# Performance work log

Measured on AMD Instinct MI355X. Metric: run time of the kernel, lower is better.

The kernel has to match this reference:

```python
import jax, jax.numpy as jnp
import numpy as np

H = 1024      # hidden_dim
NH = 16       # num_heads
HD = H // NH  # head_dim
FF = 4096     # ff_dim
EPS = 1e-6


def layer_norm(x, gamma, beta):
    # faithful to source: unbiased std (ddof=1), divide by (std + eps)
    mean = jnp.mean(x, axis=-1, keepdims=True)
    var = jnp.sum((x - mean) ** 2, axis=-1, keepdims=True) / (x.shape[-1] - 1)
    std = jnp.sqrt(var)
    return gamma * (x - mean) / (std + EPS) + beta


def linear_mulbias(x, W, b):
    # source LinearLayer: einsum('...i,io,o->...o') -> (x @ W) * b (bias MULTIPLIES)
    return jnp.einsum('bti,io->bto', x, W) * b


def setup_inputs() -> dict:
    key = jax.random.key(0)
    ks = jax.random.split(key, 11)
    B, T = 2, 2048
    return {
        'x':      jax.random.normal(ks[0], (B, T, H), jnp.float32),
        'Wqkv':   jax.random.normal(ks[1], (H, 3 * H), jnp.float32),
        'bqkv':   jax.random.normal(ks[2], (3 * H,), jnp.float32),
        'W1':     jax.random.normal(ks[3], (H, FF), jnp.float32),
        'b1':     jax.random.normal(ks[4], (FF,), jnp.float32),
        'W2':     jax.random.normal(ks[5], (FF, H), jnp.float32),
        'b2':     jax.random.normal(ks[6], (H,), jnp.float32),
        'gamma1': jax.random.normal(ks[7], (H,), jnp.float32),
        'beta1':  jax.random.normal(ks[8], (H,), jnp.float32),
        'gamma2': jax.random.normal(ks[9], (H,), jnp.float32),
        'beta2':  jax.random.normal(ks[10], (H,), jnp.float32),
    }


def attention(x, Wqkv, bqkv):
    B, T, _ = x.shape
    qkv = linear_mulbias(x, Wqkv, bqkv)                 # [B,T,3H]
    # einops 'b t (d k h) -> k b h t d' with k=3, h=NH: last dim decomposes (d,3,h)
    qkv = qkv.reshape(B, T, HD, 3, NH)
    qkv = jnp.transpose(qkv, (3, 0, 4, 1, 2))           # [3,B,NH,T,HD]
    q, k, v = qkv[0], qkv[1], qkv[2]
    scores = jnp.einsum('bhid,bhjd->bhij', q, k) / (H ** 0.5)  # scale by full hidden_dim
    attn = jax.nn.softmax(scores, axis=-1)
    out = jnp.einsum('bhij,bhjd->bhid', attn, v)        # [B,NH,T,HD]
    return jnp.transpose(out, (0, 2, 1, 3)).reshape(B, T, H)


def reference(x, Wqkv, bqkv, W1, b1, W2, b2, gamma1, beta1, gamma2, beta2):
    # dropout is identity in eval mode
    out = layer_norm(x + attention(x, Wqkv, bqkv), gamma1, beta1)
    ffn = linear_mulbias(jnp.maximum(linear_mulbias(out, W1, b1), 0.0), W2, b2)
    out = layer_norm(out + ffn, gamma2, beta2)
    return out
```

## Files before the change

kernel.cpp:

```cpp
#include <hip/hip_runtime.h>
#include <math.h>

#define B 2
#define T 2048
#define H 1024
#define NH 16
#define HD 64
#define FF 4096
#define M_TOK (B*T)
#define LOG2E 1.4426950408889634f

typedef unsigned short u16;
typedef __attribute__((ext_vector_type(8))) short bf16x8;
typedef __attribute__((ext_vector_type(4))) float f32x4;

#define WAITBAR4  asm volatile("s_waitcnt vmcnt(4)\n\ts_barrier" ::: "memory")
#define WAITBAR6  asm volatile("s_waitcnt vmcnt(6)\n\ts_barrier" ::: "memory")
#define WAITBAR0  asm volatile("s_waitcnt vmcnt(0)\n\ts_barrier" ::: "memory")

__device__ __forceinline__ u16 f2bf(float f) {
  union { float f; unsigned u; } v; v.f = f;
  const unsigned r = (v.u + 0x7FFFu + ((v.u >> 16) & 1u)) >> 16;
  return (u16)r;
}
__device__ __forceinline__ float bf2f(u16 h) {
  union { unsigned u; float f; } v; v.u = ((unsigned)h) << 16;
  return v.f;
}
__device__ __forceinline__ unsigned cvt_pk_bf16(float lo, float hi) {
  unsigned r;
  asm("v_cvt_pk_bf16_f32 %0, %1, %2" : "=v"(r) : "v"(lo), "v"(hi));
  return r;
}
__device__ __forceinline__ float m3(float a, float b, float c) {
  return fmaxf(fmaxf(a, b), c);
}
__device__ __forceinline__ void gload16(const u16* g, u16* l) {
  __builtin_amdgcn_global_load_lds(
      (const __attribute__((address_space(1))) unsigned int*)g,
      (__attribute__((address_space(3))) unsigned int*)l, 16, 0, 0);
}

__global__ __launch_bounds__(256) void split_hl(
    const float* __restrict__ in, u16* __restrict__ oh, u16* __restrict__ ol)
{
  const size_t i = ((size_t)blockIdx.x * 256 + threadIdx.x) * 4;
  const float4 v = *(const float4*)(in + i);
  union { u16 s[4]; uint2 u; } h, l;
  const float f[4] = {v.x, v.y, v.z, v.w};
#pragma unroll
  for (int j = 0; j < 4; ++j) {
    const u16 hb = f2bf(f[j]); h.s[j] = hb; l.s[j] = f2bf(f[j] - bf2f(hb));
  }
  *(uint2*)(oh + i) = h.u;
  *(uint2*)(ol + i) = l.u;
}

template<int SPLIT>
__global__ __launch_bounds__(256) void transpose_bf16(
    const float* __restrict__ in, u16* __restrict__ oh, u16* __restrict__ ol,
    int K, int N)
{
  __shared__ float tile[64][69];
  const int k0 = blockIdx.y * 64, n0 = blockIdx.x * 64;
  const int tid = threadIdx.x;
  const int r = tid >> 4, c4 = (tid & 15) * 4;
#pragma unroll
  for (int i = 0; i < 4; ++i) {
    const float4 v = *(const float4*)(in + (size_t)(k0 + i*16 + r) * N + n0 + c4);
    tile[i*16+r][c4]   = v.x; tile[i*16+r][c4+1] = v.y;
    tile[i*16+r][c4+2] = v.z; tile[i*16+r][c4+3] = v.w;
  }
  __syncthreads();
  const int n = tid >> 2, kq = tid & 3;
  union { u16 s[8]; int4 v; } ph0, ph1, pl0, pl1;
#pragma unroll
  for (int j = 0; j < 8; ++j) {
    const float f0 = tile[kq*16 + j][n];
    const float f1 = tile[kq*16 + 8 + j][n];
    const u16 h0 = f2bf(f0), h1 = f2bf(f1);
    ph0.s[j] = h0; ph1.s[j] = h1;
    if (SPLIT) { pl0.s[j] = f2bf(f0 - bf2f(h0)); pl1.s[j] = f2bf(f1 - bf2f(h1)); }
  }
  u16* po = oh + (size_t)(n0 + n) * K + k0 + kq * 16;
  *(int4*)po = ph0.v; *(int4*)(po + 8) = ph1.v;
  if (SPLIT) {
    u16* pl = ol + (size_t)(n0 + n) * K + k0 + kq * 16;
    *(int4*)pl = pl0.v; *(int4*)(pl + 8) = pl1.v;
  }
}

__device__ __forceinline__ int swz(int r, int kq) {
  return r * 32 + ((kq ^ ((r >> 1) & 3)) * 8);
}

template<int SPLIT, int RELU, int OBF, int QKV3, int DEEP3, int PARTIAL>
__global__ __launch_bounds__(256) void mfma_gemm(
    const u16* __restrict__ Ah, const u16* __restrict__ Al,
    const u16* __restrict__ Bh, const u16* __restrict__ Bl,
    const float* __restrict__ bias,
// ... 114 lines not shown
      }
      __syncthreads();
      cur = nxt;
    }
  }
#undef GSTAGE
#undef BLSTAGE

  const int orow0 = row0 + wr * 64, ocol0 = col0 + wc * 64;
#pragma unroll
  for (int n = 0; n < 4; ++n) {
    const int col = ocol0 + n * 16 + fr;
    const float bs = PARTIAL ? 1.0f : bias[col];
#pragma unroll
    for (int m = 0; m < 4; ++m) {
      const int rbase = orow0 + m * 16 + (lane >> 4) * 4;
#pragma unroll
      for (int j = 0; j < 4; ++j) {
        float v = acc[m][n][j] * bs;
        if (RELU) v = fmaxf(v, 0.0f);
        const size_t off = (size_t)(rbase + j) * N + col;
        if (OBF) Cb[off] = f2bf(v); else Cf[off] = v;
      }
    }
  }
}

__global__ __launch_bounds__(256) void repack_qkv(
    const float* __restrict__ qkv,
    u16* __restrict__ Qh, u16* __restrict__ Ql,
    u16* __restrict__ Kh, u16* __restrict__ Kl, u16* __restrict__ Vb)
{
  const int bt = blockIdx.x;
  const int b = bt >> 11, t = bt & (T - 1);
  const int tid = threadIdx.x;
  __shared__ float Ls[3 * H];
  const float* src = qkv + (size_t)bt * (3 * H);
#pragma unroll
  for (int i = 0; i < 3; ++i) {
    const int c4 = i * 256 + tid;
    *(float4*)&Ls[c4 * 4] = *(const float4*)(src + c4 * 4);
  }
  __syncthreads();
  const float qscale = LOG2E / 32.0f;
#pragma unroll
  for (int i = 0; i < 4; ++i) {
    const int j = i * 256 + tid;
    const int h = j >> 6, d = j & 63;
    const size_t dst = (((size_t)(b * NH + h)) * T + t) * HD + d;
    const float q = Ls[d * 48 + h] * qscale;
    const u16 qhb = f2bf(q);
    Qh[dst] = qhb; Ql[dst] = f2bf(q - bf2f(qhb));
    const float k = Ls[d * 48 + 16 + h];
    const u16 khb = f2bf(k);
    Kh[dst] = khb; Kl[dst] = f2bf(k - bf2f(khb));
    Vb[dst] = f2bf(Ls[d * 48 + 32 + h]);
  }
}

__global__ __launch_bounds__(256) void vtrans(
    const u16* __restrict__ Vb, u16* __restrict__ VT)
{
  __shared__ u16 Ls[64][72];
  const int bh = blockIdx.y, t0 = blockIdx.x * 64;
  const int tid = threadIdx.x;
  const int r = tid >> 2, c = (tid & 3) * 16;
  const size_t src = ((size_t)bh * T + t0 + r) * HD + c;
  *(int4*)&Ls[r][c]     = *(const int4*)(Vb + src);
  *(int4*)&Ls[r][c + 8] = *(const int4*)(Vb + src + 8);
  __syncthreads();
  const int d = tid >> 2, tc = (tid & 3) * 16;
  u16 buf[16];
#pragma unroll
  for (int i = 0; i < 16; ++i) buf[i] = Ls[tc + i][d];
  u16* dst = VT + ((size_t)bh * HD + d) * T + t0 + tc;
  *(int4*)dst       = *(int4*)&buf[0];
  *(int4*)(dst + 8) = *(int4*)&buf[8];
}

__device__ __forceinline__ int sigma_k(int r) {
  return ((r >> 5) << 5) | (((r >> 2) & 3) << 3) | (((r >> 4) & 1) << 2) | (r & 3);
}

__global__ __launch_bounds__(256) void flash_attn_mfma(
    const u16* __restrict__ Qh, const u16* __restrict__ Ql,
    const u16* __restrict__ Kh, const u16* __restrict__ Kl,
    const u16* __restrict__ VT, float* __restrict__ Out)
{
  __shared__ u16 sm[3 * 12288];
  const int i = blockIdx.x;
  const int slot = i >> 3;
  const int bh = (i & 7) * 4 + (slot >> 4);
  const int row0 = (slot & 15) * 128;
  const int b = bh >> 4, h = bh & 15;
  const int tid = threadIdx.x, wave = tid >> 6, lane = tid & 63;
  const int fr = lane & 15, kq = lane >> 4;

  bf16x8 qh[2][2], ql[2][2];
#pragma unroll
  for (int qf = 0; qf < 2; ++qf) {
    const size_t qoff = ((size_t)bh * T + row0 + wave*32 + qf*16 + fr) * HD + kq*8;
#pragma unroll
    for (int ks = 0; ks < 2; ++ks) {
      qh[qf][ks] = *(const bf16x8*)(Qh + qoff + ks*32);
      ql[qf][ks] = *(const bf16x8*)(Ql + qoff + ks*32);
    }
  }

  bf16x8 ones8;
#pragma unroll
  for (int z = 0; z < 8; ++z) ones8[z] = (short)0x3F80;

  f32x4 o[2][4] = {};
  f32x4 oex[2] = {};
  float m_[2] = {-1e30f, -1e30f};

  const int c_ = wave * 2;
  const int r0_ = c_ * 8 + (lane >> 3), s_ = lane & 7;
  const int r1_ = r0_ + 8;
  const int cd0 = s_ ^ (r0_ & 7), cd1 = s_ ^ (r1_ & 7);
  const int k0_ = sigma_k(r0_), k1_ = sigma_k(r1_);
  const u16* pKh0 = Kh + ((size_t)bh*T + k0_)*HD + cd0*8;
  const u16* pKh1 = Kh + ((size_t)bh*T + k1_)*HD + cd1*8;
  const u16* pKl0 = Kl + ((size_t)bh*T + k0_)*HD + cd0*8;
  const u16* pKl1 = Kl + ((size_t)bh*T + k1_)*HD + cd1*8;
  const u16* pV0  = VT + ((size_t)bh*HD + r0_)*T + cd0*8;
  const u16* pV1  = VT + ((size_t)bh*HD + r1_)*T + cd1*8;

#define FSTAGE(sb) do { \
    gload16(pKh0, &sm[(sb) + c_*512]);        gload16(pKh1, &sm[(sb) + (c_+1)*512]); \
    gload16(pKl0, &sm[(sb) + 4096 + c_*512]); gload16(pKl1, &sm[(sb) + 4096 + (c_+1)*512]); \
    gload16(pV0,  &sm[(sb) + 8192 + c_*512]); gload16(pV1,  &sm[(sb) + 8192 + (c_+1)*512]); \
    pKh0 += 64*HD; pKh1 += 64*HD; pKl0 += 64*HD; pKl1 += 64*HD; pV0 += 64; pV1 += 64; \
  } while (0)

  FSTAGE(0);
  FSTAGE(12288);
  WAITBAR6;
  int cslot = 0, islot = 2;

  const int NT = T / 64;
  for (int t = 0; t < NT; ++t) {
    if (t + 2 < NT) {
      FSTAGE(islot * 12288);
      islot = (islot == 2) ? 0 : islot + 1;
    }
    const u16* smb = &sm[cslot * 12288];

    f32x4 s[2][4] = {};
    __builtin_amdgcn_s_setprio(1);
#pragma unroll
    for (int ks = 0; ks < 2; ++ks) {
#pragma unroll
      for (int n = 0; n < 4; ++n) {
        const int kr = n * 16 + fr;
        const int sl = ((ks*4 + kq) ^ (kr & 7)) * 8;
        const bf16x8 kh_ = *(const bf16x8*)&smb[kr*64 + sl];
        const bf16x8 kl_ = *(const bf16x8*)&smb[4096 + kr*64 + sl];
        s[0][n] = __builtin_amdgcn_mfma_f32_16x16x32_bf16(kh_, qh[0][ks], s[0][n], 0, 0, 0);
        s[1][n] = __builtin_amdgcn_mfma_f32_16x16x32_bf16(kh_, qh[1][ks], s[1][n], 0, 0, 0);
        s[0][n] = __builtin_amdgcn_mfma_f32_16x16x32_bf16(kl_, qh[0][ks], s[0][n], 0, 0, 0);
        s[1][n] = __builtin_amdgcn_mfma_f32_16x16x32_bf16(kl_, qh[1][ks], s[1][n], 0, 0, 0);
        s[0][n] = __builtin_amdgcn_mfma_f32_16x16x32_bf16(kh_, ql[0][ks], s[0][n], 0, 0, 0);
        s[1][n] = __builtin_amdgcn_mfma_f32_16x16x32_bf16(kh_, ql[1][ks], s[1][n], 0, 0, 0);
      }
    }
    __builtin_amdgcn_s_setprio(0);

    bf16x8 vf[2][4];
#pragma unroll
    for (int ks = 0; ks < 2; ++ks)
#pragma unroll
      for (int n = 0; n < 4; ++n) {
        const int dr = n * 16 + fr;
        vf[ks][n] = *(const bf16x8*)&smb[8192 + dr*64 + (((ks*4 + kq) ^ (dr & 7)) * 8)];
      }

#pragma unroll
    for (int qf = 0; qf < 2; ++qf) {
      const float g0 = m3(s[qf][0][0], s[qf][0][1], s[qf][0][2]);
      const float g1 = m3(s[qf][0][3], s[qf][1][0], s[qf][1][1]);
      const float g2 = m3(s[qf][1][2], s[qf][1][3], s[qf][2][0]);
      const float g3 = m3(s[qf][2][1], s[qf][2][2], s[qf][2][3]);
      const float g4 = m3(s[qf][3][0], s[qf][3][1], s[qf][3][2]);
      float mx = fmaxf(m3(g0, g1, g2), m3(g3, g4, s[qf][3][3]));
      mx = fmaxf(mx, __shfl_xor(mx, 16));
      mx = fmaxf(mx, __shfl_xor(mx, 32));
      if (!__all(mx <= m_[qf] + 8.0f)) {
        const float mn = fmaxf(m_[qf], mx);
        const float fsc = exp2f(m_[qf] - mn);
        m_[qf] = mn;
#pragma unroll
        for (int n = 0; n < 4; ++n) {
          o[qf][n][0] *= fsc; o[qf][n][1] *= fsc;
          o[qf][n][2] *= fsc; o[qf][n][3] *= fsc;
        }
        oex[qf][0] *= fsc; oex[qf][1] *= fsc;
        oex[qf][2] *= fsc; oex[qf][3] *= fsc;
      }

      float p[4][4];
#pragma unroll
      for (int n = 0; n < 4; ++n)
#pragma unroll
        for (int jj = 0; jj < 4; ++jj)
          p[n][jj] = exp2f(s[qf][n][jj] - m_[qf]);

      unsigned pk[4][2];
#pragma unroll
      for (int n = 0; n < 4; ++n) {
        pk[n][0] = cvt_pk_bf16(p[n][0], p[n][1]);
        pk[n][1] = cvt_pk_bf16(p[n][2], p[n][3]);
      }
      __builtin_amdgcn_s_setprio(1);
#pragma unroll
      for (int ks = 0; ks < 2; ++ks) {
        union { unsigned u[4]; bf16x8 v; } pb;
        pb.u[0] = pk[2*ks][0];   pb.u[1] = pk[2*ks][1];
        pb.u[2] = pk[2*ks+1][0]; pb.u[3] = pk[2*ks+1][1];
#pragma unroll
        for (int n = 0; n < 4; ++n)
          o[qf][n] = __builtin_amdgcn_mfma_f32_16x16x32_bf16(vf[ks][n], pb.v, o[qf][n], 0, 0, 0);
        oex[qf] = __builtin_amdgcn_mfma_f32_16x16x32_bf16(ones8, pb.v, oex[qf], 0, 0, 0);
      }
      __builtin_amdgcn_s_setprio(0);
    }
    cslot = (cslot == 2) ? 0 : cslot + 1;
    if (t + 1 < NT) { if (t + 2 < NT) WAITBAR6; else WAITBAR0; }
  }
#undef FSTAGE

#pragma unroll
  for (int qf = 0; qf < 2; ++qf) {
    const float inv = 1.0f / oex[qf][0];
    const size_t qrow = (size_t)b * T + row0 + wave*32 + qf*16 + fr;
#pragma unroll
    for (int n = 0; n < 4; ++n) {
      float4 ov;
      ov.x = o[qf][n][0] * inv; ov.y = o[qf][n][1] * inv;
      ov.z = o[qf][n][2] * inv; ov.w = o[qf][n][3] * inv;
      *(float4*)(Out + qrow * H + h * HD + n * 16 + kq * 4) = ov;
    }
  }
}

__global__ __launch_bounds__(256) void ln_residual(
    const float* __restrict__ A, const float* __restrict__ Bz,
    const float* __restrict__ gamma, const float* __restrict__ beta,
    float* __restrict__ out, u16* __restrict__ obf)
{
  const int row = blockIdx.x, tid = threadIdx.x;
  const int wave = tid >> 6, lane = tid & 63;
  const size_t off = (size_t)row * H + tid * 4;
  const float4 av = *(const float4*)(A + off);
  const float4 bv = *(const float4*)(Bz + off);
  float4 y; y.x = av.x + bv.x; y.y = av.y + bv.y; y.z = av.z + bv.z; y.w = av.w + bv.w;
  float s  = y.x + y.y + y.z + y.w;
  float ss = y.x*y.x + y.y*y.y + y.z*y.z + y.w*y.w;
#pragma unroll
  for (int o = 32; o >= 1; o >>= 1) { s += __shfl_xor(s, o); ss += __shfl_xor(ss, o); }
  __shared__ float red[2][4];
  if (lane == 0) { red[0][wave] = s; red[1][wave] = ss; }
  __syncthreads();
  s  = red[0][0] + red[0][1] + red[0][2] + red[0][3];
  ss = red[1][0] + red[1][1] + red[1][2] + red[1][3];
  const float mean = s * (1.0f / (float)H);
  float var = (ss - (float)H * mean * mean) * (1.0f / (float)(H - 1));
  var = fmaxf(var, 0.0f);
  const float inv = 1.0f / (sqrtf(var) + 1e-6f);
  const float4 gv = *(const float4*)(gamma + tid * 4);
  const float4 be = *(const float4*)(beta + tid * 4);
  float4 o;
  o.x = gv.x * (y.x - mean) * inv + be.x;
  o.y = gv.y * (y.y - mean) * inv + be.y;
  o.z = gv.z * (y.z - mean) * inv + be.z;
  o.w = gv.w * (y.w - mean) * inv + be.w;
  *(float4*)(out + off) = o;
  if (obf) {
    union { u16 s[4]; uint2 u; } pk;
    pk.s[0] = f2bf(o.x); pk.s[1] = f2bf(o.y); pk.s[2] = f2bf(o.z); pk.s[3] = f2bf(o.w);
    *(uint2*)(obf + off) = pk.u;
  }
}

__global__ __launch_bounds__(256) void ln_residual_sk(
    const float* __restrict__ A, const float* __restrict__ PA,
    const float* __restrict__ PB, const float* __restrict__ bb,
    const float* __restrict__ gamma, const float* __restrict__ beta,
    float* __restrict__ out)
{
  const int row = blockIdx.x, tid = threadIdx.x;
  const int wave = tid >> 6, lane = tid & 63;
  const size_t off = (size_t)row * H + tid * 4;
  const float4 av = *(const float4*)(A + off);
  const float4 pa = *(const float4*)(PA + off);
  const float4 pb = *(const float4*)(PB + off);
  const float4 bw = *(const float4*)(bb + tid * 4);
  float4 y;
  y.x = av.x + (pa.x + pb.x) * bw.x;
  y.y = av.y + (pa.y + pb.y) * bw.y;
  y.z = av.z + (pa.z + pb.z) * bw.z;
  y.w = av.w + (pa.w + pb.w) * bw.w;
  float s  = y.x + y.y + y.z + y.w;
  float ss = y.x*y.x + y.y*y.y + y.z*y.z + y.w*y.w;
#pragma unroll
  for (int o = 32; o >= 1; o >>= 1) { s += __shfl_xor(s, o); ss += __shfl_xor(ss, o); }
  __shared__ float red[2][4];
  if (lane == 0) { red[0][wave] = s; red[1][wave] = ss; }
  __syncthreads();
  s  = red[0][0] + red[0][1] + red[0][2] + red[0][3];
  ss = red[1][0] + red[1][1] + red[1][2] + red[1][3];
  const float mean = s * (1.0f / (float)H);
  float var = (ss - (float)H * mean * mean) * (1.0f / (float)(H - 1));
  var = fmaxf(var, 0.0f);
  const float inv = 1.0f / (sqrtf(var) + 1e-6f);
  const float4 gv = *(const float4*)(gamma + tid * 4);
  const float4 be = *(const float4*)(beta + tid * 4);
  float4 o;
  o.x = gv.x * (y.x - mean) * inv + be.x;
  o.y = gv.y * (y.y - mean) * inv + be.y;
  o.z = gv.z * (y.z - mean) * inv + be.z;
  o.w = gv.w * (y.w - mean) * inv + be.w;
  *(float4*)(out + off) = o;
}

extern "C" void kernel_launch(void* const* d_in, const int* in_sizes, int n_in,
                              void* d_out, int out_size, void* d_ws, size_t ws_size,
                              hipStream_t stream)
{
  const float* x    = (const float*)d_in[0];
  const float* Wqkv = (const float*)d_in[1];
  const float* bqkv = (const float*)d_in[2];
  const float* W1   = (const float*)d_in[3];
  const float* b1   = (const float*)d_in[4];
  const float* W2   = (const float*)d_in[5];
  const float* b2   = (const float*)d_in[6];
  const float* g1   = (const float*)d_in[7];
  const float* be1  = (const float*)d_in[8];
  const float* g2   = (const float*)d_in[9];
  const float* be2  = (const float*)d_in[10];
  float* out = (float*)d_out;
  char* w = (char*)d_ws;

  float* qkv  = (float*)(w + 0);
  u16*   h1b  = (u16*)  (w + 0);
  u16*   W1T  = (u16*)  (w + 35651584);
  u16*   W2T  = (u16*)  (w + 44040192);
  u16*   xh   = (u16*)  (w + 52428800);
  u16*   xl   = (u16*)  (w + 60817408);
  u16*   Qh   = (u16*)  (w + 52428800);
  u16*   Ql   = (u16*)  (w + 60817408);
  u16*   WqTh = (u16*)  (w + 69206016);
  u16*   WqTl = (u16*)  (w + 75497472);
  u16*   Khb  = (u16*)  (w + 69206016);
  u16*   Klb  = (u16*)  (w + 77594624);
  u16*   Vbb  = (u16*)  (w + 85983232);
  u16*   VTb  = (u16*)  (w + 94371840);
  float* pAB  = (float*)(w + 52428800);
  float* attn = (float*)(w + 102760448);
  float* ln1  = (float*)(w + 119537664);
  u16*   ln1b = (u16*)  (w + 136314880);

  split_hl<<<4096, 256, 0, stream>>>(x, xh, xl);
  transpose_bf16<1><<<dim3(48, 16), 256, 0, stream>>>(Wqkv, WqTh, WqTl, H, 3*H);
  mfma_gemm<1,0,0,1,0,0><<<24 * 32, 256, 0, stream>>>(xh, xl, WqTh, WqTl, bqkv,
                                                      qkv, nullptr, M_TOK, 3*H, H);
  repack_qkv<<<M_TOK, 256, 0, stream>>>(qkv, Qh, Ql, Khb, Klb, Vbb);
  vtrans<<<dim3(T/64, B*NH), 256, 0, stream>>>(Vbb, VTb);
  flash_attn_mfma<<<512, 256, 0, stream>>>(Qh, Ql, Khb, Klb, VTb, attn);
  ln_residual<<<M_TOK, 256, 0, stream>>>(x, attn, g1, be1, ln1, ln1b);
  transpose_bf16<0><<<dim3(64, 16), 256, 0, stream>>>(W1, W1T, nullptr, H, FF);
  mfma_gemm<0,1,1,0,1,0><<<32 * 32, 256, 0, stream>>>(ln1b, nullptr, W1T, nullptr, b1,
                                                      nullptr, h1b, M_TOK, FF, H);
  transpose_bf16<0><<<dim3(16, 64), 256, 0, stream>>>(W2, W2T, nullptr, FF, H);
  mfma_gemm<0,0,0,0,1,1><<<dim3(8 * 32, 2), 256, 0, stream>>>(h1b, nullptr, W2T, nullptr, nullptr,
                                                              pAB, nullptr, M_TOK, H, FF);
  ln_residual_sk<<<M_TOK, 256, 0, stream>>>(ln1, pAB, pAB + 4194304, b2, g2, be2, out);
}
```

Before: 315.4 us.

## Split flash attention work across 8 waves with 16 query rows each

The flash attention kernel now launches 512 threads per block, and each of the 8 waves handles one 16-row query fragment instead of two. Every wave loads one K/V row chunk per stage instead of two, and the barrier wait counts are adjusted to match. Per-wave register state (Q fragments, accumulators, scores) is halved, and the launch bounds ask for more waves per CU so latency can be hidden better. In exchange, each K/V fragment read from shared memory now feeds half as many MFMAs, which raises LDS read traffic per FLOP.

```diff
diff --git a/kernel.cpp b/kernel.cpp
--- a/kernel.cpp
+++ b/kernel.cpp
@@ -14,8 +14,8 @@
 typedef __attribute__((ext_vector_type(8))) short bf16x8;
 typedef __attribute__((ext_vector_type(4))) float f32x4;
 
+#define WAITBAR3  asm volatile("s_waitcnt vmcnt(3)\n\ts_barrier" ::: "memory")
 #define WAITBAR4  asm volatile("s_waitcnt vmcnt(4)\n\ts_barrier" ::: "memory")
-#define WAITBAR6  asm volatile("s_waitcnt vmcnt(6)\n\ts_barrier" ::: "memory")
 #define WAITBAR0  asm volatile("s_waitcnt vmcnt(0)\n\ts_barrier" ::: "memory")
 
 __device__ __forceinline__ u16 f2bf(float f) {
@@ -296,7 +296,7 @@
   return ((r >> 5) << 5) | (((r >> 2) & 3) << 3) | (((r >> 4) & 1) << 2) | (r & 3);
 }
 
-__global__ __launch_bounds__(256) void flash_attn_mfma(
+__global__ __launch_bounds__(512, 4) void flash_attn_mfma(
     const u16* __restrict__ Qh, const u16* __restrict__ Ql,
     const u16* __restrict__ Kh, const u16* __restrict__ Kl,
     const u16* __restrict__ VT, float* __restrict__ Out)
@@ -310,47 +310,40 @@
   const int tid = threadIdx.x, wave = tid >> 6, lane = tid & 63;
   const int fr = lane & 15, kq = lane >> 4;
 
-  bf16x8 qh[2][2], ql[2][2];
-#pragma unroll
-  for (int qf = 0; qf < 2; ++qf) {
-    const size_t qoff = ((size_t)bh * T + row0 + wave*32 + qf*16 + fr) * HD + kq*8;
-#pragma unroll
-    for (int ks = 0; ks < 2; ++ks) {
-      qh[qf][ks] = *(const bf16x8*)(Qh + qoff + ks*32);
-      ql[qf][ks] = *(const bf16x8*)(Ql + qoff + ks*32);
-    }
+  bf16x8 qh[2], ql[2];
+  const size_t qoff = ((size_t)bh * T + row0 + wave*16 + fr) * HD + kq*8;
+#pragma unroll
+  for (int ks = 0; ks < 2; ++ks) {
+    qh[ks] = *(const bf16x8*)(Qh + qoff + ks*32);
+    ql[ks] = *(const bf16x8*)(Ql + qoff + ks*32);
   }
 
   bf16x8 ones8;
 #pragma unroll
   for (int z = 0; z < 8; ++z) ones8[z] = (short)0x3F80;
 
-  f32x4 o[2][4] = {};
-  f32x4 oex[2] = {};
-  float m_[2] = {-1e30f, -1e30f};
-
-  const int c_ = wave * 2;
+  f32x4 o[4] = {};
+  f32x4 oex = {};
+  float m_ = -1e30f;
+
+  const int c_ = wave;
   const int r0_ = c_ * 8 + (lane >> 3), s_ = lane & 7;
-  const int r1_ = r0_ + 8;
-  const int cd0 = s_ ^ (r0_ & 7), cd1 = s_ ^ (r1_ & 7);
-  const int k0_ = sigma_k(r0_), k1_ = sigma_k(r1_);
+  const int cd0 = s_ ^ (r0_ & 7);
+  const int k0_ = sigma_k(r0_);
   const u16* pKh0 = Kh + ((size_t)bh*T + k0_)*HD + cd0*8;
-  const u16* pKh1 = Kh + ((size_t)bh*T + k1_)*HD + cd1*8;
   const u16* pKl0 = Kl + ((size_t)bh*T + k0_)*HD + cd0*8;
-  const u16* pKl1 = Kl + ((size_t)bh*T + k1_)*HD + cd1*8;
   const u16* pV0  = VT + ((size_t)bh*HD + r0_)*T + cd0*8;
-  const u16* pV1  = VT + ((size_t)bh*HD + r1_)*T + cd1*8;
 
 #define FSTAGE(sb) do { \
-    gload16(pKh0, &sm[(sb) + c_*512]);        gload16(pKh1, &sm[(sb) + (c_+1)*512]); \
-    gload16(pKl0, &sm[(sb) + 4096 + c_*512]); gload16(pKl1, &sm[(sb) + 4096 + (c_+1)*512]); \
-    gload16(pV0,  &sm[(sb) + 8192 + c_*512]); gload16(pV1,  &sm[(sb) + 8192 + (c_+1)*512]); \
-    pKh0 += 64*HD; pKh1 += 64*HD; pKl0 += 64*HD; pKl1 += 64*HD; pV0 += 64; pV1 += 64; \
+    gload16(pKh0, &sm[(sb) + c_*512]); \
+    gload16(pKl0, &sm[(sb) + 4096 + c_*512]); \
+    gload16(pV0,  &sm[(sb) + 8192 + c_*512]); \
+    pKh0 += 64*HD; pKl0 += 64*HD; pV0 += 64; \
   } while (0)
 
   FSTAGE(0);
   FSTAGE(12288);
-  WAITBAR6;
+  WAITBAR3;
   int cslot = 0, islot = 2;
 
   const int NT = T / 64;
@@ -361,7 +354,7 @@
     }
     const u16* smb = &sm[cslot * 12288];
 
-    f32x4 s[2][4] = {};
+    f32x4 s[4] = {};
     __builtin_amdgcn_s_setprio(1);
 #pragma unroll
     for (int ks = 0; ks < 2; ++ks) {
@@ -371,88 +364,76 @@
         const int sl = ((ks*4 + kq) ^ (kr & 7)) * 8;
         const bf16x8 kh_ = *(const bf16x8*)&smb[kr*64 + sl];
         const bf16x8 kl_ = *(const bf16x8*)&smb[4096 + kr*64 + sl];
-        s[0][n] = __builtin_amdgcn_mfma_f32_16x16x32_bf16(kh_, qh[0][ks], s[0][n], 0, 0, 0);
-        s[1][n] = __builtin_amdgcn_mfma_f32_16x16x32_bf16(kh_, qh[1][ks], s[1][n], 0, 0, 0);
-        s[0][n] = __builtin_amdgcn_mfma_f32_16x16x32_bf16(kl_, qh[0][ks], s[0][n], 0, 0, 0);
-        s[1][n] = __builtin_amdgcn_mfma_f32_16x16x32_bf16(kl_, qh[1][ks], s[1][n], 0, 0, 0);
-        s[0][n] = __builtin_amdgcn_mfma_f32_16x16x32_bf16(kh_, ql[0][ks], s[0][n], 0, 0, 0);
-        s[1][n] = __builtin_amdgcn_mfma_f32_16x16x32_bf16(kh_, ql[1][ks], s[1][n], 0, 0, 0);
+        s[n] = __builtin_amdgcn_mfma_f32_16x16x32_bf16(kh_, qh[ks], s[n], 0, 0, 0);
+        s[n] = __builtin_amdgcn_mfma_f32_16x16x32_bf16(kl_, qh[ks], s[n], 0, 0, 0);
+        s[n] = __builtin_amdgcn_mfma_f32_16x16x32_bf16(kh_, ql[ks], s[n], 0, 0, 0);
       }
     }
     __builtin_amdgcn_s_setprio(0);
 
-    bf16x8 vf[2][4];
-#pragma unroll
-    for (int ks = 0; ks < 2; ++ks)
+    const float g0 = m3(s[0][0], s[0][1], s[0][2]);
+    const float g1 = m3(s[0][3], s[1][0], s[1][1]);
+    const float g2 = m3(s[1][2], s[1][3], s[2][0]);
+    const float g3 = m3(s[2][1], s[2][2], s[2][3]);
+    const float g4 = m3(s[3][0], s[3][1], s[3][2]);
+    float mx = fmaxf(m3(g0, g1, g2), m3(g3, g4, s[3][3]));
+    mx = fmaxf(mx, __shfl_xor(mx, 16));
+    mx = fmaxf(mx, __shfl_xor(mx, 32));
+    if (!__all(mx <= m_ + 8.0f)) {
+      const float mn = fmaxf(m_, mx);
+      const float fsc = exp2f(m_ - mn);
+      m_ = mn;
+#pragma unroll
+      for (int n = 0; n < 4; ++n) {
+        o[n][0] *= fsc; o[n][1] *= fsc;
+        o[n][2] *= fsc; o[n][3] *= fsc;
+      }
+      oex[0] *= fsc; oex[1] *= fsc; oex[2] *= fsc; oex[3] *= fsc;
+    }
+
+    float p[4][4];
+#pragma unroll
+    for (int n = 0; n < 4; ++n)
+#pragma unroll
+      for (int jj = 0; jj < 4; ++jj)
+        p[n][jj] = exp2f(s[n][jj] - m_);
+
+    unsigned pk[4][2];
+#pragma unroll
+    for (int n = 0; n < 4; ++n) {
+      pk[n][0] = cvt_pk_bf16(p[n][0], p[n][1]);
+      pk[n][1] = cvt_pk_bf16(p[n][2], p[n][3]);
+    }
+
+    __builtin_amdgcn_s_setprio(1);
+#pragma unroll
+    for (int ks = 0; ks < 2; ++ks) {
+      union { unsigned u[4]; bf16x8 v; } pb;
+      pb.u[0] = pk[2*ks][0];   pb.u[1] = pk[2*ks][1];
+      pb.u[2] = pk[2*ks+1][0]; pb.u[3] = pk[2*ks+1][1];
 #pragma unroll
       for (int n = 0; n < 4; ++n) {
         const int dr = n * 16 + fr;
-        vf[ks][n] = *(const bf16x8*)&smb[8192 + dr*64 + (((ks*4 + kq) ^ (dr & 7)) * 8)];
-      }
-
-#pragma unroll
-    for (int qf = 0; qf < 2; ++qf) {
-      const float g0 = m3(s[qf][0][0], s[qf][0][1], s[qf][0][2]);
-      const float g1 = m3(s[qf][0][3], s[qf][1][0], s[qf][1][1]);
-      const float g2 = m3(s[qf][1][2], s[qf][1][3], s[qf][2][0]);
-      const float g3 = m3(s[qf][2][1], s[qf][2][2], s[qf][2][3]);
-      const float g4 = m3(s[qf][3][0], s[qf][3][1], s[qf][3][2]);
-      float mx = fmaxf(m3(g0, g1, g2), m3(g3, g4, s[qf][3][3]));
-      mx = fmaxf(mx, __shfl_xor(mx, 16));
-      mx = fmaxf(mx, __shfl_xor(mx, 32));
-      if (!__all(mx <= m_[qf] + 8.0f)) {
-        const float mn = fmaxf(m_[qf], mx);
-        const float fsc = exp2f(m_[qf] - mn);
-        m_[qf] = mn;
-#pragma unroll
-        for (int n = 0; n < 4; ++n) {
-          o[qf][n][0] *= fsc; o[qf][n][1] *= fsc;
-          o[qf][n][2] *= fsc; o[qf][n][3] *= fsc;
-        }
-        oex[qf][0] *= fsc; oex[qf][1] *= fsc;
-        oex[qf][2] *= fsc; oex[qf][3] *= fsc;
-      }
-
-      float p[4][4];
-#pragma unroll
-      for (int n = 0; n < 4; ++n)
-#pragma unroll
-        for (int jj = 0; jj < 4; ++jj)
-          p[n][jj] = exp2f(s[qf][n][jj] - m_[qf]);
-
-      unsigned pk[4][2];
-#pragma unroll
-      for (int n = 0; n < 4; ++n) {
-        pk[n][0] = cvt_pk_bf16(p[n][0], p[n][1]);
-        pk[n][1] = cvt_pk_bf16(p[n][2], p[n][3]);
-      }
-      __builtin_amdgcn_s_setprio(1);
-#pragma unroll
-      for (int ks = 0; ks < 2; ++ks) {
-        union { unsigned u[4]; bf16x8 v; } pb;
-        pb.u[0] = pk[2*ks][0];   pb.u[1] = pk[2*ks][1];
-        pb.u[2] = pk[2*ks+1][0]; pb.u[3] = pk[2*ks+1][1];
-#pragma unroll
-        for (int n = 0; n < 4; ++n)
-          o[qf][n] = __builtin_amdgcn_mfma_f32_16x16x32_bf16(vf[ks][n], pb.v, o[qf][n], 0, 0, 0);
-        oex[qf] = __builtin_amdgcn_mfma_f32_16x16x32_bf16(ones8, pb.v, oex[qf], 0, 0, 0);
-      }
-      __builtin_amdgcn_s_setprio(0);
-    }
+        const bf16x8 vf = *(const bf16x8*)&smb[8192 + dr*64 + (((ks*4 + kq) ^ (dr & 7)) * 8)];
+        o[n] = __builtin_amdgcn_mfma_f32_16x16x32_bf16(vf, pb.v, o[n], 0, 0, 0);
+      }
+      oex = __builtin_amdgcn_mfma_f32_16x16x32_bf16(ones8, pb.v, oex, 0, 0, 0);
+    }
+    __builtin_amdgcn_s_setprio(0);
+
     cslot = (cslot == 2) ? 0 : cslot + 1;
-    if (t + 1 < NT) { if (t + 2 < NT) WAITBAR6; else WAITBAR0; }
+    if (t + 1 < NT) { if (t + 2 < NT) WAITBAR3; else WAITBAR0; }
   }
 #undef FSTAGE
 
-#pragma unroll
-  for (int qf = 0; qf < 2; ++qf) {
-    const float inv = 1.0f / oex[qf][0];
-    const size_t qrow = (size_t)b * T + row0 + wave*32 + qf*16 + fr;
+  {
+    const float inv = 1.0f / oex[0];
+    const size_t qrow = (size_t)b * T + row0 + wave*16 + fr;
 #pragma unroll
     for (int n = 0; n < 4; ++n) {
       float4 ov;
-      ov.x = o[qf][n][0] * inv; ov.y = o[qf][n][1] * inv;
-      ov.z = o[qf][n][2] * inv; ov.w = o[qf][n][3] * inv;
+      ov.x = o[n][0] * inv; ov.y = o[n][1] * inv;
+      ov.z = o[n][2] * inv; ov.w = o[n][3] * inv;
       *(float4*)(Out + qrow * H + h * HD + n * 16 + kq * 4) = ov;
     }
   }
@@ -581,7 +562,7 @@
                                                       qkv, nullptr, M_TOK, 3*H, H);
   repack_qkv<<<M_TOK, 256, 0, stream>>>(qkv, Qh, Ql, Khb, Klb, Vbb);
   vtrans<<<dim3(T/64, B*NH), 256, 0, stream>>>(Vbb, VTb);
-  flash_attn_mfma<<<512, 256, 0, stream>>>(Qh, Ql, Khb, Klb, VTb, attn);
+  flash_attn_mfma<<<512, 512, 0, stream>>>(Qh, Ql, Khb, Klb, VTb, attn);
   ln_residual<<<M_TOK, 256, 0, stream>>>(x, attn, g1, be1, ln1, ln1b);
   transpose_bf16<0><<<dim3(64, 16), 256, 0, stream>>>(W1, W1T, nullptr, H, FF);
   mfma_gemm<0,1,1,0,1,0><<<32 * 32, 256, 0, stream>>>(ln1b, nullptr, W1T, nullptr, b1,
```

Result: faster. 305.9 us (-3.0%).

## Split flash attention over KV halves with 512-thread blocks and merge in LayerNorm

Applied to the files above, without the earlier changes.

Flash attention now uses 512-thread blocks covering 256 query rows each, and the KV sequence is split into two halves across blockIdx.y. Each half writes unnormalized partial outputs plus its row max and sum to workspace. The following LayerNorm kernel merges the two partials with log-sum-exp rescaling before adding the residual. This is meant to change occupancy and parallelism in the attention kernel, at the cost of extra partial-output traffic and a merge step.

```diff
diff --git a/kernel.cpp b/kernel.cpp
--- a/kernel.cpp
+++ b/kernel.cpp
@@ -14,8 +14,8 @@
 typedef __attribute__((ext_vector_type(8))) short bf16x8;
 typedef __attribute__((ext_vector_type(4))) float f32x4;
 
+#define WAITBAR3  asm volatile("s_waitcnt vmcnt(3)\n\ts_barrier" ::: "memory")
 #define WAITBAR4  asm volatile("s_waitcnt vmcnt(4)\n\ts_barrier" ::: "memory")
-#define WAITBAR6  asm volatile("s_waitcnt vmcnt(6)\n\ts_barrier" ::: "memory")
 #define WAITBAR0  asm volatile("s_waitcnt vmcnt(0)\n\ts_barrier" ::: "memory")
 
 __device__ __forceinline__ u16 f2bf(float f) {
@@ -296,17 +296,18 @@
   return ((r >> 5) << 5) | (((r >> 2) & 3) << 3) | (((r >> 4) & 1) << 2) | (r & 3);
 }
 
-__global__ __launch_bounds__(256) void flash_attn_mfma(
+__global__ __launch_bounds__(512, 4) void flash_attn_mfma(
     const u16* __restrict__ Qh, const u16* __restrict__ Ql,
     const u16* __restrict__ Kh, const u16* __restrict__ Kl,
-    const u16* __restrict__ VT, float* __restrict__ Out)
+    const u16* __restrict__ VT, float* __restrict__ Pp,
+    float* __restrict__ Ms, float* __restrict__ Lsum)
 {
   __shared__ u16 sm[3 * 12288];
   const int i = blockIdx.x;
+  const int hf = blockIdx.y;
   const int slot = i >> 3;
-  const int bh = (i & 7) * 4 + (slot >> 4);
-  const int row0 = (slot & 15) * 128;
-  const int b = bh >> 4, h = bh & 15;
+  const int bh = (i & 7) * 4 + (slot >> 3);
+  const int row0 = (slot & 7) * 256;
   const int tid = threadIdx.x, wave = tid >> 6, lane = tid & 63;
   const int fr = lane & 15, kq = lane >> 4;
 
@@ -329,31 +330,28 @@
   f32x4 oex[2] = {};
   float m_[2] = {-1e30f, -1e30f};
 
-  const int c_ = wave * 2;
+  const int c_ = wave;
   const int r0_ = c_ * 8 + (lane >> 3), s_ = lane & 7;
-  const int r1_ = r0_ + 8;
-  const int cd0 = s_ ^ (r0_ & 7), cd1 = s_ ^ (r1_ & 7);
-  const int k0_ = sigma_k(r0_), k1_ = sigma_k(r1_);
-  const u16* pKh0 = Kh + ((size_t)bh*T + k0_)*HD + cd0*8;
-  const u16* pKh1 = Kh + ((size_t)bh*T + k1_)*HD + cd1*8;
-  const u16* pKl0 = Kl + ((size_t)bh*T + k0_)*HD + cd0*8;
-  const u16* pKl1 = Kl + ((size_t)bh*T + k1_)*HD + cd1*8;
-  const u16* pV0  = VT + ((size_t)bh*HD + r0_)*T + cd0*8;
-  const u16* pV1  = VT + ((size_t)bh*HD + r1_)*T + cd1*8;
+  const int cd0 = s_ ^ (r0_ & 7);
+  const int k0_ = sigma_k(r0_);
+  const int kvbase = hf * (T / 2);
+  const u16* pKh0 = Kh + ((size_t)bh*T + kvbase + k0_)*HD + cd0*8;
+  const u16* pKl0 = Kl + ((size_t)bh*T + kvbase + k0_)*HD + cd0*8;
+  const u16* pV0  = VT + ((size_t)bh*HD + r0_)*T + kvbase + cd0*8;
 
 #define FSTAGE(sb) do { \
-    gload16(pKh0, &sm[(sb) + c_*512]);        gload16(pKh1, &sm[(sb) + (c_+1)*512]); \
-    gload16(pKl0, &sm[(sb) + 4096 + c_*512]); gload16(pKl1, &sm[(sb) + 4096 + (c_+1)*512]); \
-    gload16(pV0,  &sm[(sb) + 8192 + c_*512]); gload16(pV1,  &sm[(sb) + 8192 + (c_+1)*512]); \
-    pKh0 += 64*HD; pKh1 += 64*HD; pKl0 += 64*HD; pKl1 += 64*HD; pV0 += 64; pV1 += 64; \
+    gload16(pKh0, &sm[(sb) + c_*512]); \
+    gload16(pKl0, &sm[(sb) + 4096 + c_*512]); \
+    gload16(pV0,  &sm[(sb) + 8192 + c_*512]); \
+    pKh0 += 64*HD; pKl0 += 64*HD; pV0 += 64; \
   } while (0)
 
   FSTAGE(0);
   FSTAGE(12288);
-  WAITBAR6;
+  WAITBAR3;
   int cslot = 0, islot = 2;
 
-  const int NT = T / 64;
+  const int NT = (T / 2) / 64;
   for (int t = 0; t < NT; ++t) {
     if (t + 2 < NT) {
       FSTAGE(islot * 12288);
@@ -440,35 +438,52 @@
       __builtin_amdgcn_s_setprio(0);
     }
     cslot = (cslot == 2) ? 0 : cslot + 1;
-    if (t + 1 < NT) { if (t + 2 < NT) WAITBAR6; else WAITBAR0; }
+    if (t + 1 < NT) { if (t + 2 < NT) WAITBAR3; else WAITBAR0; }
   }
 #undef FSTAGE
 
+  const size_t pbase = ((size_t)hf * (B*NH) + bh) * T;
 #pragma unroll
   for (int qf = 0; qf < 2; ++qf) {
-    const float inv = 1.0f / oex[qf][0];
-    const size_t qrow = (size_t)b * T + row0 + wave*32 + qf*16 + fr;
+    const size_t qrow = pbase + row0 + wave*32 + qf*16 + fr;
 #pragma unroll
     for (int n = 0; n < 4; ++n) {
       float4 ov;
-      ov.x = o[qf][n][0] * inv; ov.y = o[qf][n][1] * inv;
-      ov.z = o[qf][n][2] * inv; ov.w = o[qf][n][3] * inv;
-      *(float4*)(Out + qrow * H + h * HD + n * 16 + kq * 4) = ov;
-    }
-  }
-}
-
-__global__ __launch_bounds__(256) void ln_residual(
-    const float* __restrict__ A, const float* __restrict__ Bz,
+      ov.x = o[qf][n][0]; ov.y = o[qf][n][1];
+      ov.z = o[qf][n][2]; ov.w = o[qf][n][3];
+      *(float4*)(Pp + qrow * HD + n * 16 + kq * 4) = ov;
+    }
+    if (kq == 0) { Ms[qrow] = m_[qf]; Lsum[qrow] = oex[qf][0]; }
+  }
+}
+
+__global__ __launch_bounds__(256) void ln_residual_att(
+    const float* __restrict__ A, const float* __restrict__ Pp,
+    const float* __restrict__ Ms, const float* __restrict__ Lsum,
     const float* __restrict__ gamma, const float* __restrict__ beta,
     float* __restrict__ out, u16* __restrict__ obf)
 {
   const int row = blockIdx.x, tid = threadIdx.x;
   const int wave = tid >> 6, lane = tid & 63;
+  const int b = row >> 11, t = row & (T - 1);
+  const int h = tid >> 4;
+  const int d = (tid & 15) * 4;
+  const size_t s0 = ((size_t)(b * NH + h)) * T + t;
+  const size_t s1 = s0 + (size_t)(B * NH) * T;
+  const float m0v = Ms[s0], m1v = Ms[s1];
+  const float l0v = Lsum[s0], l1v = Lsum[s1];
+  const float Mf = fmaxf(m0v, m1v);
+  const float w0 = exp2f(m0v - Mf), w1 = exp2f(m1v - Mf);
+  const float invl = 1.0f / (l0v * w0 + l1v * w1);
+  const float4 o0 = *(const float4*)(Pp + s0 * HD + d);
+  const float4 o1 = *(const float4*)(Pp + s1 * HD + d);
   const size_t off = (size_t)row * H + tid * 4;
   const float4 av = *(const float4*)(A + off);
-  const float4 bv = *(const float4*)(Bz + off);
-  float4 y; y.x = av.x + bv.x; y.y = av.y + bv.y; y.z = av.z + bv.z; y.w = av.w + bv.w;
+  float4 y;
+  y.x = av.x + (o0.x * w0 + o1.x * w1) * invl;
+  y.y = av.y + (o0.y * w0 + o1.y * w1) * invl;
+  y.z = av.z + (o0.z * w0 + o1.z * w1) * invl;
+  y.w = av.w + (o0.w * w0 + o1.w * w1) * invl;
   float s  = y.x + y.y + y.z + y.w;
   float ss = y.x*y.x + y.y*y.y + y.z*y.z + y.w*y.w;
 #pragma unroll
@@ -557,6 +572,9 @@
   char* w = (char*)d_ws;
 
   float* qkv  = (float*)(w + 0);
+  float* Pp   = (float*)(w + 0);
+  float* Msb  = (float*)(w + 33554432);
+  float* Lsb  = (float*)(w + 34078720);
   u16*   h1b  = (u16*)  (w + 0);
   u16*   W1T  = (u16*)  (w + 35651584);
   u16*   W2T  = (u16*)  (w + 44040192);
@@ -571,7 +589,6 @@
   u16*   Vbb  = (u16*)  (w + 85983232);
   u16*   VTb  = (u16*)  (w + 94371840);
   float* pAB  = (float*)(w + 52428800);
-  float* attn = (float*)(w + 102760448);
   float* ln1  = (float*)(w + 119537664);
   u16*   ln1b = (u16*)  (w + 136314880);
 
@@ -581,8 +598,9 @@
                                                       qkv, nullptr, M_TOK, 3*H, H);
   repack_qkv<<<M_TOK, 256, 0, stream>>>(qkv, Qh, Ql, Khb, Klb, Vbb);
   vtrans<<<dim3(T/64, B*NH), 256, 0, stream>>>(Vbb, VTb);
-  flash_attn_mfma<<<512, 256, 0, stream>>>(Qh, Ql, Khb, Klb, VTb, attn);
-  ln_residual<<<M_TOK, 256, 0, stream>>>(x, attn, g1, be1, ln1, ln1b);
+  flash_attn_mfma<<<dim3(256, 2), 512, 0, stream>>>(Qh, Ql, Khb, Klb, VTb,
+                                                    Pp, Msb, Lsb);
+  ln_residual_att<<<M_TOK, 256, 0, stream>>>(x, Pp, Msb, Lsb, g1, be1, ln1, ln1b);
   transpose_bf16<0><<<dim3(64, 16), 256, 0, stream>>>(W1, W1T, nullptr, H, FF);
   mfma_gemm<0,1,1,0,1,0><<<32 * 32, 256, 0, stream>>>(ln1b, nullptr, W1T, nullptr, b1,
                                                       nullptr, h1b, M_TOK, FF, H);
```

Result: slower. 358.8 us (+13.8%).

## Split flash attention KV range across two wave groups with in-block merge

Applied to the files above, without the earlier changes.

Doubles the flash-attention block to 512 threads: two groups of four waves each process half of the key/value sequence for the same 128 query rows, using 32-key tiles per stage. At the end, group 1 writes its partial output, running max and row sum to shared memory, and group 0 merges the two online-softmax states and writes the result. The aim is more waves in flight per CU to hide latency, at the cost of a final merge step, a smaller per-iteration tile and higher register pressure under the new launch bounds.

```diff
diff --git a/kernel.cpp b/kernel.cpp
--- a/kernel.cpp
+++ b/kernel.cpp
@@ -14,8 +14,8 @@
 typedef __attribute__((ext_vector_type(8))) short bf16x8;
 typedef __attribute__((ext_vector_type(4))) float f32x4;
 
+#define WAITBAR3  asm volatile("s_waitcnt vmcnt(3)\n\ts_barrier" ::: "memory")
 #define WAITBAR4  asm volatile("s_waitcnt vmcnt(4)\n\ts_barrier" ::: "memory")
-#define WAITBAR6  asm volatile("s_waitcnt vmcnt(6)\n\ts_barrier" ::: "memory")
 #define WAITBAR0  asm volatile("s_waitcnt vmcnt(0)\n\ts_barrier" ::: "memory")
 
 __device__ __forceinline__ u16 f2bf(float f) {
@@ -296,7 +296,7 @@
   return ((r >> 5) << 5) | (((r >> 2) & 3) << 3) | (((r >> 4) & 1) << 2) | (r & 3);
 }
 
-__global__ __launch_bounds__(256) void flash_attn_mfma(
+__global__ __launch_bounds__(512, 4) void flash_attn_mfma(
     const u16* __restrict__ Qh, const u16* __restrict__ Ql,
     const u16* __restrict__ Kh, const u16* __restrict__ Kl,
     const u16* __restrict__ VT, float* __restrict__ Out)
@@ -309,11 +309,12 @@
   const int b = bh >> 4, h = bh & 15;
   const int tid = threadIdx.x, wave = tid >> 6, lane = tid & 63;
   const int fr = lane & 15, kq = lane >> 4;
+  const int u = wave & 3, grp = wave >> 2;
 
   bf16x8 qh[2][2], ql[2][2];
 #pragma unroll
   for (int qf = 0; qf < 2; ++qf) {
-    const size_t qoff = ((size_t)bh * T + row0 + wave*32 + qf*16 + fr) * HD + kq*8;
+    const size_t qoff = ((size_t)bh * T + row0 + u*32 + qf*16 + fr) * HD + kq*8;
 #pragma unroll
     for (int ks = 0; ks < 2; ++ks) {
       qh[qf][ks] = *(const bf16x8*)(Qh + qoff + ks*32);
@@ -329,48 +330,59 @@
   f32x4 oex[2] = {};
   float m_[2] = {-1e30f, -1e30f};
 
-  const int c_ = wave * 2;
-  const int r0_ = c_ * 8 + (lane >> 3), s_ = lane & 7;
-  const int r1_ = r0_ + 8;
-  const int cd0 = s_ ^ (r0_ & 7), cd1 = s_ ^ (r1_ & 7);
-  const int k0_ = sigma_k(r0_), k1_ = sigma_k(r1_);
-  const u16* pKh0 = Kh + ((size_t)bh*T + k0_)*HD + cd0*8;
-  const u16* pKh1 = Kh + ((size_t)bh*T + k1_)*HD + cd1*8;
-  const u16* pKl0 = Kl + ((size_t)bh*T + k0_)*HD + cd0*8;
-  const u16* pKl1 = Kl + ((size_t)bh*T + k1_)*HD + cd1*8;
-  const u16* pV0  = VT + ((size_t)bh*HD + r0_)*T + cd0*8;
-  const u16* pV1  = VT + ((size_t)bh*HD + r1_)*T + cd1*8;
+  const int kb0 = grp * (T / 2);
+  const u16* sp0; const u16* sp1; const u16* sp2;
+  int so0, so1, so2, st0, st1, st2;
+#define MKCH(J, SP, SO, ST) do { \
+    const int sub_ = u * 3 + (J); \
+    if (sub_ < 8) { \
+      const int r_ = (sub_ & 3) * 8 + (lane >> 3); \
+      const int cd_ = (lane & 7) ^ (r_ & 7); \
+      const u16* base_ = (sub_ < 4) ? Kh : Kl; \
+      SP = base_ + ((size_t)bh * T + kb0 + sigma_k(r_)) * HD + cd_ * 8; \
+      ST = 32 * HD; \
+    } else { \
+      const int r_ = (sub_ & 3) * 16 + (lane >> 2); \
+      const int cd_ = (lane & 3) ^ (r_ & 3); \
+      SP = VT + ((size_t)bh * HD + r_) * T + kb0 + cd_ * 8; \
+      ST = 32; \
+    } \
+    SO = grp * 6144 + sub_ * 512; \
+  } while (0)
+  MKCH(0, sp0, so0, st0);
+  MKCH(1, sp1, so1, st1);
+  MKCH(2, sp2, so2, st2);
+#undef MKCH
 
 #define FSTAGE(sb) do { \
-    gload16(pKh0, &sm[(sb) + c_*512]);        gload16(pKh1, &sm[(sb) + (c_+1)*512]); \
-    gload16(pKl0, &sm[(sb) + 4096 + c_*512]); gload16(pKl1, &sm[(sb) + 4096 + (c_+1)*512]); \
-    gload16(pV0,  &sm[(sb) + 8192 + c_*512]); gload16(pV1,  &sm[(sb) + 8192 + (c_+1)*512]); \
-    pKh0 += 64*HD; pKh1 += 64*HD; pKl0 += 64*HD; pKl1 += 64*HD; pV0 += 64; pV1 += 64; \
+    gload16(sp0, &sm[(sb) + so0]); sp0 += st0; \
+    gload16(sp1, &sm[(sb) + so1]); sp1 += st1; \
+    gload16(sp2, &sm[(sb) + so2]); sp2 += st2; \
   } while (0)
 
   FSTAGE(0);
   FSTAGE(12288);
-  WAITBAR6;
+  WAITBAR3;
   int cslot = 0, islot = 2;
 
-  const int NT = T / 64;
+  const int NT = 32;
   for (int t = 0; t < NT; ++t) {
     if (t + 2 < NT) {
       FSTAGE(islot * 12288);
       islot = (islot == 2) ? 0 : islot + 1;
     }
-    const u16* smb = &sm[cslot * 12288];
-
-    f32x4 s[2][4] = {};
+    const u16* gb = &sm[cslot * 12288 + grp * 6144];
+
+    f32x4 s[2][2] = {};
     __builtin_amdgcn_s_setprio(1);
 #pragma unroll
     for (int ks = 0; ks < 2; ++ks) {
 #pragma unroll
-      for (int n = 0; n < 4; ++n) {
+      for (int n = 0; n < 2; ++n) {
         const int kr = n * 16 + fr;
         const int sl = ((ks*4 + kq) ^ (kr & 7)) * 8;
-        const bf16x8 kh_ = *(const bf16x8*)&smb[kr*64 + sl];
-        const bf16x8 kl_ = *(const bf16x8*)&smb[4096 + kr*64 + sl];
+        const bf16x8 kh_ = *(const bf16x8*)&gb[kr*64 + sl];
+        const bf16x8 kl_ = *(const bf16x8*)&gb[2048 + kr*64 + sl];
         s[0][n] = __builtin_amdgcn_mfma_f32_16x16x32_bf16(kh_, qh[0][ks], s[0][n], 0, 0, 0);
         s[1][n] = __builtin_amdgcn_mfma_f32_16x16x32_bf16(kh_, qh[1][ks], s[1][n], 0, 0, 0);
         s[0][n] = __builtin_amdgcn_mfma_f32_16x16x32_bf16(kl_, qh[0][ks], s[0][n], 0, 0, 0);
@@ -381,23 +393,19 @@
     }
     __builtin_amdgcn_s_setprio(0);
 
-    bf16x8 vf[2][4];
-#pragma unroll
-    for (int ks = 0; ks < 2; ++ks)
-#pragma unroll
-      for (int n = 0; n < 4; ++n) {
-        const int dr = n * 16 + fr;
-        vf[ks][n] = *(const bf16x8*)&smb[8192 + dr*64 + (((ks*4 + kq) ^ (dr & 7)) * 8)];
-      }
+    bf16x8 vf[4];
+#pragma unroll
+    for (int dn = 0; dn < 4; ++dn) {
+      const int dr = dn * 16 + fr;
+      vf[dn] = *(const bf16x8*)&gb[4096 + dr*32 + ((kq ^ (dr & 3)) * 8)];
+    }
 
 #pragma unroll
     for (int qf = 0; qf < 2; ++qf) {
-      const float g0 = m3(s[qf][0][0], s[qf][0][1], s[qf][0][2]);
-      const float g1 = m3(s[qf][0][3], s[qf][1][0], s[qf][1][1]);
-      const float g2 = m3(s[qf][1][2], s[qf][1][3], s[qf][2][0]);
-      const float g3 = m3(s[qf][2][1], s[qf][2][2], s[qf][2][3]);
-      const float g4 = m3(s[qf][3][0], s[qf][3][1], s[qf][3][2]);
-      float mx = fmaxf(m3(g0, g1, g2), m3(g3, g4, s[qf][3][3]));
+      const float f1 = m3(s[qf][0][0], s[qf][0][1], s[qf][0][2]);
+      const float f2 = m3(s[qf][0][3], s[qf][1][0], s[qf][1][1]);
+      const float f3 = m3(s[qf][1][2], s[qf][1][3], f1);
+      float mx = fmaxf(f2, f3);
       mx = fmaxf(mx, __shfl_xor(mx, 16));
       mx = fmaxf(mx, __shfl_xor(mx, 32));
       if (!__all(mx <= m_[qf] + 8.0f)) {
@@ -405,55 +413,75 @@
         const float fsc = exp2f(m_[qf] - mn);
         m_[qf] = mn;
 #pragma unroll
-        for (int n = 0; n < 4; ++n) {
-          o[qf][n][0] *= fsc; o[qf][n][1] *= fsc;
-          o[qf][n][2] *= fsc; o[qf][n][3] *= fsc;
+        for (int dn = 0; dn < 4; ++dn) {
+          o[qf][dn][0] *= fsc; o[qf][dn][1] *= fsc;
+          o[qf][dn][2] *= fsc; o[qf][dn][3] *= fsc;
         }
         oex[qf][0] *= fsc; oex[qf][1] *= fsc;
         oex[qf][2] *= fsc; oex[qf][3] *= fsc;
       }
 
-      float p[4][4];
-#pragma unroll
-      for (int n = 0; n < 4; ++n)
+      float p[2][4];
+#pragma unroll
+      for (int n = 0; n < 2; ++n)
 #pragma unroll
         for (int jj = 0; jj < 4; ++jj)
           p[n][jj] = exp2f(s[qf][n][jj] - m_[qf]);
 
-      unsigned pk[4][2];
-#pragma unroll
-      for (int n = 0; n < 4; ++n) {
-        pk[n][0] = cvt_pk_bf16(p[n][0], p[n][1]);
-        pk[n][1] = cvt_pk_bf16(p[n][2], p[n][3]);
-      }
+      union { unsigned pu[4]; bf16x8 v; } pb;
+      pb.pu[0] = cvt_pk_bf16(p[0][0], p[0][1]);
+      pb.pu[1] = cvt_pk_bf16(p[0][2], p[0][3]);
+      pb.pu[2] = cvt_pk_bf16(p[1][0], p[1][1]);
+      pb.pu[3] = cvt_pk_bf16(p[1][2], p[1][3]);
+
       __builtin_amdgcn_s_setprio(1);
 #pragma unroll
-      for (int ks = 0; ks < 2; ++ks) {
-        union { unsigned u[4]; bf16x8 v; } pb;
-        pb.u[0] = pk[2*ks][0];   pb.u[1] = pk[2*ks][1];
-        pb.u[2] = pk[2*ks+1][0]; pb.u[3] = pk[2*ks+1][1];
-#pragma unroll
-        for (int n = 0; n < 4; ++n)
-          o[qf][n] = __builtin_amdgcn_mfma_f32_16x16x32_bf16(vf[ks][n], pb.v, o[qf][n], 0, 0, 0);
-        oex[qf] = __builtin_amdgcn_mfma_f32_16x16x32_bf16(ones8, pb.v, oex[qf], 0, 0, 0);
-      }
+      for (int dn = 0; dn < 4; ++dn)
+        o[qf][dn] = __builtin_amdgcn_mfma_f32_16x16x32_bf16(vf[dn], pb.v, o[qf][dn], 0, 0, 0);
+      oex[qf] = __builtin_amdgcn_mfma_f32_16x16x32_bf16(ones8, pb.v, oex[qf], 0, 0, 0);
       __builtin_amdgcn_s_setprio(0);
     }
     cslot = (cslot == 2) ? 0 : cslot + 1;
-    if (t + 1 < NT) { if (t + 2 < NT) WAITBAR6; else WAITBAR0; }
+    if (t + 1 < NT) { if (t + 2 < NT) WAITBAR3; else WAITBAR0; }
   }
 #undef FSTAGE
 
-#pragma unroll
-  for (int qf = 0; qf < 2; ++qf) {
-    const float inv = 1.0f / oex[qf][0];
-    const size_t qrow = (size_t)b * T + row0 + wave*32 + qf*16 + fr;
-#pragma unroll
-    for (int n = 0; n < 4; ++n) {
-      float4 ov;
-      ov.x = o[qf][n][0] * inv; ov.y = o[qf][n][1] * inv;
-      ov.z = o[qf][n][2] * inv; ov.w = o[qf][n][3] * inv;
-      *(float4*)(Out + qrow * H + h * HD + n * 16 + kq * 4) = ov;
+  __syncthreads();
+  float* fm = (float*)sm;
+  const int rb_ = u * 2176;
+  if (grp == 1) {
+#pragma unroll
+    for (int qf = 0; qf < 2; ++qf) {
+#pragma unroll
+      for (int dn = 0; dn < 4; ++dn)
+        *(f32x4*)&fm[rb_ + (qf*4 + dn)*256 + lane*4] = o[qf][dn];
+      if (kq == 0) {
+        fm[rb_ + 2048 + qf*16 + fr] = m_[qf];
+        fm[rb_ + 2080 + qf*16 + fr] = oex[qf][0];
+      }
+    }
+  }
+  __syncthreads();
+  if (grp == 0) {
+#pragma unroll
+    for (int qf = 0; qf < 2; ++qf) {
+      const float mB = fm[rb_ + 2048 + qf*16 + fr];
+      const float lB = fm[rb_ + 2080 + qf*16 + fr];
+      const float M  = fmaxf(m_[qf], mB);
+      const float wA = exp2f(m_[qf] - M);
+      const float wB = exp2f(mB - M);
+      const float inv = 1.0f / (oex[qf][0] * wA + lB * wB);
+      const size_t qrow = (size_t)b * T + row0 + u*32 + qf*16 + fr;
+#pragma unroll
+      for (int dn = 0; dn < 4; ++dn) {
+        const f32x4 ob = *(const f32x4*)&fm[rb_ + (qf*4 + dn)*256 + lane*4];
+        float4 ov;
+        ov.x = (o[qf][dn][0] * wA + ob[0] * wB) * inv;
+        ov.y = (o[qf][dn][1] * wA + ob[1] * wB) * inv;
+        ov.z = (o[qf][dn][2] * wA + ob[2] * wB) * inv;
+        ov.w = (o[qf][dn][3] * wA + ob[3] * wB) * inv;
+        *(float4*)(Out + qrow * H + h * HD + dn * 16 + kq * 4) = ov;
+      }
     }
   }
 }
@@ -581,7 +609,7 @@
                                                       qkv, nullptr, M_TOK, 3*H, H);
   repack_qkv<<<M_TOK, 256, 0, stream>>>(qkv, Qh, Ql, Khb, Klb, Vbb);
   vtrans<<<dim3(T/64, B*NH), 256, 0, stream>>>(Vbb, VTb);
-  flash_attn_mfma<<<512, 256, 0, stream>>>(Qh, Ql, Khb, Klb, VTb, attn);
+  flash_attn_mfma<<<512, 512, 0, stream>>>(Qh, Ql, Khb, Klb, VTb, attn);
   ln_residual<<<M_TOK, 256, 0, stream>>>(x, attn, g1, be1, ln1, ln1b);
   transpose_bf16<0><<<dim3(64, 16), 256, 0, stream>>>(W1, W1T, nullptr, H, FF);
   mfma_gemm<0,1,1,0,1,0><<<32 * 32, 256, 0, stream>>>(ln1b, nullptr, W1T, nullptr, b1,
```

New measurement: 319.7 us. Within noise of the previous version (+1.4%).
